# Kernel tuning notes

Hardware: AMD Instinct MI355X
Metric: run time of the kernel (lower is better)

The kernel has to match this reference:

```python
import jax, jax.numpy as jnp
import numpy as np

N = 50000          # nodes
E = 1000000        # edges
EMB = 64           # emb_dim
L = 3              # num_layer
B = 250            # graphs (200 nodes each)
XF, EF = 7, 5      # node / edge feature dims
BN_EPS = 1e-5


def setup_inputs() -> dict:
    key = jax.random.key(0)
    ks = jax.random.split(key, 16)
    x = jax.random.normal(ks[0], (N, XF), dtype=jnp.float32)
    edge_attr = jax.random.normal(ks[1], (E, EF), dtype=jnp.float32)
    edge_index = jax.random.randint(ks[2], (2, E), 0, N, dtype=jnp.int32)
    # 250 contiguous graphs of 200 nodes: last node index of each graph
    last_idx = jnp.arange(1, B + 1, dtype=jnp.int32) * (N // B) - 1
    s = 0.05
    xW = jax.random.normal(ks[3], (XF, EMB), dtype=jnp.float32) * s
    xb = jnp.zeros((EMB,), dtype=jnp.float32)
    eW = jax.random.normal(ks[4], (L, EF, EMB), dtype=jnp.float32) * s
    eb = jnp.zeros((L, EMB), dtype=jnp.float32)
    W1 = jax.random.normal(ks[5], (L, EMB, 2 * EMB), dtype=jnp.float32) * s
    b1 = jnp.zeros((L, 2 * EMB), dtype=jnp.float32)
    W2 = jax.random.normal(ks[6], (L, 2 * EMB, EMB), dtype=jnp.float32) * s
    b2 = jnp.zeros((L, EMB), dtype=jnp.float32)
    gamma = jnp.ones((L, EMB), dtype=jnp.float32)
    beta = jnp.zeros((L, EMB), dtype=jnp.float32)
    return {"x": x, "edge_attr": edge_attr, "edge_index": edge_index,
            "last_idx": last_idx, "xW": xW, "xb": xb, "eW": eW, "eb": eb,
            "W1": W1, "b1": b1, "W2": W2, "b2": b2,
            "gamma": gamma, "beta": beta}


def _gnn_forward(x, edge_attr, edge_index, last_idx, xW, xb, eW, eb, W1, b1, W2, b2, gamma, beta):
    n = x.shape[0]
    # self-loop edge attrs: first column = 8, rest 0
    self_attr = jnp.zeros((n, EF), dtype=edge_attr.dtype).at[:, 0].set(8.0)
    ea = jnp.concatenate([edge_attr, self_attr], axis=0)          # [E+N, EF]
    loop = jnp.arange(n, dtype=edge_index.dtype)
    src = jnp.concatenate([edge_index[0], loop])                  # x_j indices
    dst = jnp.concatenate([edge_index[1], loop])                  # aggregation targets

    h = x @ xW + xb                                               # [N, EMB]
    for l in range(L):
        e = ea @ eW[l] + eb[l]                                    # [E+N, EMB]
        msg = h[src] + e                                          # gather + combine
        agg = jax.ops.segment_sum(msg, dst, num_segments=n)       # scatter-add
        h2 = jax.nn.relu(agg @ W1[l] + b1[l]) @ W2[l] + b2[l]     # GIN MLP
        mean = jnp.mean(h2, axis=0)
        var = jnp.mean(jnp.square(h2 - mean), axis=0)             # biased, like torch BN
        hn = (h2 - mean) * jax.lax.rsqrt(var + BN_EPS) * gamma[l] + beta[l]
        h = jax.nn.elu(hn) if l < L - 1 else hn                   # drop_ratio = 0
    return h[last_idx]                                            # super-node reps [B, EMB]


def reference(x, edge_attr, edge_index, last_idx, xW, xb, eW, eb, W1, b1, W2, b2, gamma, beta):
    return _gnn_forward(x, edge_attr, edge_index, last_idx, xW, xb, eW, eb, W1, b1, W2, b2, gamma, beta)
```

## Files before the change

kernel.cpp:

```cpp
#include <hip/hip_runtime.h>

#define N_NODES 50000
#define N_EDGES 1000000
#define EMB     64
#define HID     128
#define NLAYER  3
#define NGRAPH  250
#define XFD     7
#define EFD     5
#define BN_EPS  1e-5f

#define BKT_SH 8
#define BKT_SZ 256
#define NBKT   ((N_NODES + BKT_SZ - 1) / BKT_SZ)
#define CHKE   4096
#define NCHK   ((N_EDGES + CHKE - 1) / CHKE)
#define CNTM   (NBKT * NCHK)
#define NB2    ((CNTM + 255) / 256)

typedef short bf8_t __attribute__((ext_vector_type(8)));
typedef float f4_t  __attribute__((ext_vector_type(4)));

union FragU {
    uint4 q;
    bf8_t v;
    unsigned short u[8];
};

__device__ __forceinline__ void atomAddF(float* p, float v) {
    __hip_atomic_fetch_add(p, v, __ATOMIC_RELAXED, __HIP_MEMORY_SCOPE_AGENT);
}

__device__ __forceinline__ unsigned short f2bf(float f) {
    unsigned int u = __float_as_uint(f);
    u += 0x7fffu + ((u >> 16) & 1u);
    return (unsigned short)(u >> 16);
}
__device__ __forceinline__ float bf2f(unsigned short s) {
    return __uint_as_float(((unsigned int)s) << 16);
}
__device__ __forceinline__ float4 bf4(ushort4 u) {
    return make_float4(bf2f(u.x), bf2f(u.y), bf2f(u.z), bf2f(u.w));
}

__global__ void k_input(const float* __restrict__ x, const float* __restrict__ xW,
                        const float* __restrict__ xb, unsigned short* __restrict__ h) {
    int gid = blockIdx.x * 256 + threadIdx.x;
    if (gid >= (N_NODES + 1) * EMB) return;
    int n = gid >> 6, f = gid & 63;
    if (n == N_NODES) { h[gid] = 0; return; }
    float acc = xb[f];
#pragma unroll
    for (int k = 0; k < XFD; ++k) acc = fmaf(x[n * XFD + k], xW[k * EMB + f], acc);
    h[gid] = f2bf(acc);
}

__global__ void k_packW(const float* __restrict__ W1, const float* __restrict__ W2,
                        unsigned short* __restrict__ pw1, unsigned short* __restrict__ pw2) {
    int gid = blockIdx.x * 256 + threadIdx.x;
    int layer = gid >> 14;
    int r = gid & 16383;
    if (layer >= NLAYER) return;
    if (r < 8192) {
        int p = r;
        int j = p & 7, lane = (p >> 3) & 63, ts = p >> 9;
        int t = ts >> 1, s = ts & 1;
        int k = 32 * s + 8 * (lane >> 4) + j;
        int n = 16 * t + (lane & 15);
        pw1[layer * 8192 + p] = f2bf(W1[layer * EMB * HID + k * HID + n]);
    } else {
        int p = r - 8192;
        int j = p & 7, lane = (p >> 3) & 63, ts = p >> 9;
        int t = ts >> 2, s = ts & 3;
        int k = 32 * s + 8 * (lane >> 4) + j;
        int n = 16 * t + (lane & 15);
        pw2[layer * 8192 + p] = f2bf(W2[layer * HID * EMB + k * EMB + n]);
    }
}

__global__ __launch_bounds__(256) void k_binA(const int* __restrict__ dst,
                                              int* __restrict__ cntmat) {
    __shared__ int hist[NBKT];
    int tid = threadIdx.x, c = blockIdx.x;
    for (int i = tid; i < NBKT; i += 256) hist[i] = 0;
    __syncthreads();
    int e0 = c * CHKE, e1 = min(e0 + CHKE, N_EDGES);
    for (int i = e0 + tid; i < e1; i += 256) atomicAdd(&hist[dst[i] >> BKT_SH], 1);
    __syncthreads();
    for (int b = tid; b < NBKT; b += 256) cntmat[b * NCHK + c] = hist[b];
}

__global__ __launch_bounds__(256) void k_gscanA(const int* __restrict__ in, int n,
                                                int* __restrict__ bsum) {
    int tid = threadIdx.x, lane = tid & 63, wid = tid >> 6;
    int i = blockIdx.x * 256 + tid;
    int v = (i < n) ? in[i] : 0;
#pragma unroll
    for (int off = 32; off; off >>= 1) v += __shfl_down(v, off);
    __shared__ int ws[4];
    if (lane == 0) ws[wid] = v;
    __syncthreads();
    if (tid == 0) bsum[blockIdx.x] = ws[0] + ws[1] + ws[2] + ws[3];
}

__global__ __launch_bounds__(256) void k_gscanB(const int* __restrict__ bsum, int nb,
                                                int* __restrict__ boff) {
    int tid = threadIdx.x, lane = tid & 63, wid = tid >> 6;
    int v = (tid < nb) ? bsum[tid] : 0;
    int x = v;
#pragma unroll
    for (int off = 1; off < 64; off <<= 1) {
        int y = __shfl_up(x, off);
        if (lane >= off) x += y;
    }
    __shared__ int wtot[4];
    if (lane == 63) wtot[wid] = x;
    __syncthreads();
    int woff = 0;
    for (int w = 0; w < wid; ++w) woff += wtot[w];
    if (tid < nb) boff[tid] = woff + x - v;
}

__global__ __launch_bounds__(256) void k_gscanC(const int* __restrict__ in, int n,
                                                const int* __restrict__ boff,
                                                int* __restrict__ out) {
    int tid = threadIdx.x, lane = tid & 63, wid = tid >> 6;
    int i = blockIdx.x * 256 + tid;
    int v = (i < n) ? in[i] : 0;
    int x = v;
#pragma unroll
    for (int off = 1; off < 64; off <<= 1) {
        int y = __shfl_up(x, off);
        if (lane >= off) x += y;
    }
    __shared__ int wtot[4];
    if (lane == 63) wtot[wid] = x;
    __syncthreads();
    int woff = boff[blockIdx.x];
    for (int w = 0; w < wid; ++w) woff += wtot[w];
    if (i < n) out[i] = woff + x - v;
}

__global__ __launch_bounds__(256) void k_binC(const int* __restrict__ src,
                                              const int* __restrict__ dst,
                                              const int* __restrict__ off2,
                                              int2* __restrict__ bufSD) {
    __shared__ int cur[NBKT];
    int tid = threadIdx.x, c = blockIdx.x;
    for (int b = tid; b < NBKT; b += 256) cur[b] = off2[b * NCHK + c];
    __syncthreads();
    int e0 = c * CHKE, e1 = min(e0 + CHKE, N_EDGES);
    for (int i = e0 + tid; i < e1; i += 256) {
        int d = dst[i];
        int b = d >> BKT_SH;
        int p = atomicAdd(&cur[b], 1);
        bufSD[p] = make_int2(src[i], ((d & (BKT_SZ - 1)) << 20) | i);
    }
}

__global__ __launch_bounds__(256) void k_binD(const int2* __restrict__ bufSD,
                                              const int* __restrict__ off2,
                                              int* __restrict__ csr,
                                              int* __restrict__ csrE,
                                              int* __restrict__ rowstart) {
    __shared__ int hist[BKT_SZ];
    __shared__ int cur[BKT_SZ];
    __shared__ int wtot[4];
    int tid = threadIdx.x, b = blockIdx.x;
    int bstart = off2[b * NCHK];
    int bend = (b + 1 < NBKT) ? off2[(b + 1) * NCHK] : N_EDGES;
    hist[tid] = 0;
    __syncthreads();
    for (int j = bstart + tid; j < bend; j += 256)
        atomicAdd(&hist[bufSD[j].y >> 20], 1);
    __syncthreads();
    int lane = tid & 63, wid = tid >> 6;
    int v = hist[tid], x = v;
#pragma unroll
    for (int off = 1; off < 64; off <<= 1) {
        int y = __shfl_up(x, off);
        if (lane >= off) x += y;
    }
    if (lane == 63) wtot[wid] = x;
    __syncthreads();
    int woff = 0;
    for (int w = 0; w < wid; ++w) woff += wtot[w];
    int ex = woff + x - v;
    cur[tid] = ex;
    int node = b * BKT_SZ + tid;
    if (node < N_NODES) rowstart[node] = bstart + ex;
    if (b == NBKT - 1 && tid == 0) rowstart[N_NODES] = N_EDGES;
    __syncthreads();
    for (int j = bstart + tid; j < bend; j += 256) {
        int2 t = bufSD[j];
        int local = t.y >> 20;
        int p = atomicAdd(&cur[local], 1);
        csr[bstart + p] = t.x;
        csrE[bstart + p] = t.y & 0xFFFFF;
    }
}

__global__ __launch_bounds__(256) void k_aggE(const int* __restrict__ rowstart,
                                              const int* __restrict__ csrE,
                                              const float* __restrict__ ea,
                                              float* __restrict__ aggE) {
    int wave = (blockIdx.x * 256 + threadIdx.x) >> 6;
    int lane = threadIdx.x & 63;
    int g = lane >> 4, l15 = lane & 15;
    int n = wave * 4 + g;
    if (n >= N_NODES) return;
    int j0 = rowstart[n], j1 = rowstart[n + 1];
    float s0 = 0.f, s1 = 0.f, s2 = 0.f, s3 = 0.f, s4 = 0.f;
    for (int j = j0 + l15; j < j1; j += 16) {
        int e = csrE[j];
        const float* p = ea + (size_t)e * EFD;
        s0 += p[0]; s1 += p[1]; s2 += p[2]; s3 += p[3]; s4 += p[4];
    }
#pragma unroll
    for (int off = 1; off < 16; off <<= 1) {
        s0 += __shfl_xor(s0, off);
        s1 += __shfl_xor(s1, off);
        s2 += __shfl_xor(s2, off);
        s3 += __shfl_xor(s3, off);
        s4 += __shfl_xor(s4, off);
    }
    if (l15 < 5) {
        float v = (l15 == 0) ? s0 : (l15 == 1) ? s1 : (l15 == 2) ? s2
                : (l15 == 3) ? s3 : s4;
        aggE[(size_t)n * EFD + l15] = v;
    }
}

#define ACC8(v)                                                         \
    do {                                                                \
        f0 += __uint_as_float((v).x << 16);                             \
        f1 += __uint_as_float((v).x & 0xffff0000u);                     \
        f2 += __uint_as_float((v).y << 16);                             \
        f3 += __uint_as_float((v).y & 0xffff0000u);                     \
        f4 += __uint_as_float((v).z << 16);                             \
        f5 += __uint_as_float((v).z & 0xffff0000u);                     \
        f6 += __uint_as_float((v).w << 16);                             \
        f7 += __uint_as_float((v).w & 0xffff0000u);                     \
    } while (0)

__global__ __launch_bounds__(256) void k_agg(const unsigned short* __restrict__ h,
                                             float* __restrict__ agg,
                                             const int* __restrict__ rowstart,
                                             const int* __restrict__ csr,
                                             const float* __restrict__ aggE,
                                             const float* __restrict__ eWl,
                                             const float* __restrict__ ebl) {
    int wave = (blockIdx.x * 256 + threadIdx.x) >> 6;
    int lane = threadIdx.x & 63;
    int nbase = wave * 4;
    if (nbase >= N_NODES) return;
    int lg3 = lane >> 3, lq3 = lane & 7;
    int lg = lane >> 4, lq = lane & 15;
    const uint4* hb8 = (const uint4*)h;
    const ushort4* hb4 = (const ushort4*)h;
    const float4* eW4 = (const float4*)eWl;
    float4 ew0 = eW4[lq], ew1 = eW4[16 + lq], ew2 = eW4[32 + lq],
           ew3 = eW4[48 + lq], ew4 = eW4[64 + lq];
    float4 eb4 = ((const float4*)ebl)[lq];
    int nend = min(nbase + 4, N_NODES);
    for (int n = nbase; n < nend; ++n) {
        int j0 = rowstart[n], j1 = rowstart[n + 1];
        float f0 = 0.f, f1 = 0.f, f2 = 0.f, f3 = 0.f,
              f4 = 0.f, f5 = 0.f, f6 = 0.f, f7 = 0.f;
        for (int j = j0; j < j1;) {
            int take = j1 - j;
            if (take > 64) take = 64;
            int myid = (lane < take) ? csr[j + lane] : N_NODES;
            int s0 = __shfl(myid, lg3);
            int s1 = __shfl(myid, 8 + lg3);
            int s2 = __shfl(myid, 16 + lg3);
            int s3 = __shfl(myid, 24 + lg3);
            uint4 v0 = hb8[(size_t)s0 * 8 + lq3];
            uint4 v1 = hb8[(size_t)s1 * 8 + lq3];
            uint4 v2 = hb8[(size_t)s2 * 8 + lq3];
            uint4 v3 = hb8[(size_t)s3 * 8 + lq3];
            ACC8(v0); ACC8(v1); ACC8(v2); ACC8(v3);
            if (take > 32) {
                int s4 = __shfl(myid, 32 + lg3);
                int s5 = __shfl(myid, 40 + lg3);
                int s6 = __shfl(myid, 48 + lg3);
                int s7 = __shfl(myid, 56 + lg3);
                uint4 w0 = hb8[(size_t)s4 * 8 + lq3];
                uint4 w1 = hb8[(size_t)s5 * 8 + lq3];
                uint4 w2 = hb8[(size_t)s6 * 8 + lq3];
                uint4 w3 = hb8[(size_t)s7 * 8 + lq3];
                ACC8(w0); ACC8(w1); ACC8(w2); ACC8(w3);
            }
            j += take;
        }
#define RED8(F)                     \
        F += __shfl_xor(F, 8);      \
        F += __shfl_xor(F, 16);     \
        F += __shfl_xor(F, 32);
        RED8(f0) RED8(f1) RED8(f2) RED8(f3) RED8(f4) RED8(f5) RED8(f6) RED8(f7)
#undef RED8
        int srcl = lq >> 1;
        float x0 = __shfl(f0, srcl), x4 = __shfl(f4, srcl);
        float x1 = __shfl(f1, srcl), x5 = __shfl(f5, srcl);
        float x2 = __shfl(f2, srcl), x6 = __shfl(f6, srcl);
        float x3 = __shfl(f3, srcl), x7 = __shfl(f7, srcl);
        bool hiHalf = (lq & 1) != 0;
        float4 acc;
        acc.x = hiHalf ? x4 : x0;
        acc.y = hiHalf ? x5 : x1;
        acc.z = hiHalf ? x6 : x2;
        acc.w = hiHalf ? x7 : x3;
        float a0 = aggE[n * 5 + 0], a1 = aggE[n * 5 + 1], a2 = aggE[n * 5 + 2],
              a3 = aggE[n * 5 + 3], a4 = aggE[n * 5 + 4];
        float c0 = a0 + 8.f;
        float ce = (float)(j1 - j0) + 1.f;
        float4 bb = bf4(hb4[(size_t)n * 16 + lq]);
        bb.x = fmaf(c0, ew0.x, bb.x); bb.y = fmaf(c0, ew0.y, bb.y);
        bb.z = fmaf(c0, ew0.z, bb.z); bb.w = fmaf(c0, ew0.w, bb.w);
        bb.x = fmaf(a1, ew1.x, bb.x); bb.y = fmaf(a1, ew1.y, bb.y);
        bb.z = fmaf(a1, ew1.z, bb.z); bb.w = fmaf(a1, ew1.w, bb.w);
        bb.x = fmaf(a2, ew2.x, bb.x); bb.y = fmaf(a2, ew2.y, bb.y);
        bb.z = fmaf(a2, ew2.z, bb.z); bb.w = fmaf(a2, ew2.w, bb.w);
        bb.x = fmaf(a3, ew3.x, bb.x); bb.y = fmaf(a3, ew3.y, bb.y);
        bb.z = fmaf(a3, ew3.z, bb.z); bb.w = fmaf(a3, ew3.w, bb.w);
        bb.x = fmaf(a4, ew4.x, bb.x); bb.y = fmaf(a4, ew4.y, bb.y);
        bb.z = fmaf(a4, ew4.z, bb.z); bb.w = fmaf(a4, ew4.w, bb.w);
        bb.x = fmaf(ce, eb4.x, bb.x); bb.y = fmaf(ce, eb4.y, bb.y);
        bb.z = fmaf(ce, eb4.z, bb.z); bb.w = fmaf(ce, eb4.w, bb.w);
        if (lg == 0) {
            ((float4*)agg)[(size_t)n * 16 + lq] =
                make_float4(acc.x + bb.x, acc.y + bb.y, acc.z + bb.z, acc.w + bb.w);
        }
    }
}
#undef ACC8

__global__ __launch_bounds__(256) void k_mlp(const float* __restrict__ agg,
                                             float* __restrict__ h2,
                                             const unsigned short* __restrict__ pw1,
                                             const float* __restrict__ b1l,
                                             const unsigned short* __restrict__ pw2,
                                             const float* __restrict__ b2l,
                                             float* __restrict__ stats) {
    __shared__ __align__(16) unsigned short hid[64 * 136];
    int tid = threadIdx.x;
    int w = tid >> 6, lane = tid & 63;
    int q = lane >> 4, l15 = lane & 15;
    int n0 = blockIdx.x * 64;
    int mrow = n0 + 16 * w + l15;
    const float* arow = agg + (size_t)(mrow < N_NODES ? mrow : N_NODES - 1) * EMB;
    FragU fa[2];
#pragma unroll
    for (int s = 0; s < 2; ++s) {
        float4 x0 = *(const float4*)&arow[32 * s + 8 * q];
        float4 x1 = *(const float4*)&arow[32 * s + 8 * q + 4];
        fa[s].u[0] = f2bf(x0.x); fa[s].u[1] = f2bf(x0.y);
        fa[s].u[2] = f2bf(x0.z); fa[s].u[3] = f2bf(x0.w);
        fa[s].u[4] = f2bf(x1.x); fa[s].u[5] = f2bf(x1.y);
        fa[s].u[6] = f2bf(x1.z); fa[s].u[7] = f2bf(x1.w);
    }
    const uint4* w1f = (const uint4*)pw1;
    f4_t acc1[8];
#pragma unroll
    for (int t = 0; t < 8; ++t) {
        acc1[t] = (f4_t){0.f, 0.f, 0.f, 0.f};
        FragU b0, b1;
        b0.q = w1f[(t * 2 + 0) * 64 + lane];
        b1.q = w1f[(t * 2 + 1) * 64 + lane];
        acc1[t] = __builtin_amdgcn_mfma_f32_16x16x32_bf16(fa[0].v, b0.v, acc1[t], 0, 0, 0);
        acc1[t] = __builtin_amdgcn_mfma_f32_16x16x32_bf16(fa[1].v, b1.v, acc1[t], 0, 0, 0);
    }
#pragma unroll
    for (int t = 0; t < 8; ++t) {
        int col = 16 * t + l15;
        float bv = b1l[col];
#pragma unroll
        for (int r = 0; r < 4; ++r) {
            int m = 16 * w + q * 4 + r;
            hid[m * 136 + col] = f2bf(fmaxf(acc1[t][r] + bv, 0.f));
        }
    }
    FragU fa2[4];
#pragma unroll
    for (int s = 0; s < 4; ++s)
        fa2[s].q = *(const uint4*)&hid[(16 * w + l15) * 136 + 32 * s + 8 * q];
    const uint4* w2f = (const uint4*)pw2;
    f4_t acc2[4];
#pragma unroll
    for (int t = 0; t < 4; ++t) {
        acc2[t] = (f4_t){0.f, 0.f, 0.f, 0.f};
#pragma unroll
        for (int s = 0; s < 4; ++s) {
            FragU b;
            b.q = w2f[(t * 4 + s) * 64 + lane];
            acc2[t] = __builtin_amdgcn_mfma_f32_16x16x32_bf16(fa2[s].v, b.v, acc2[t], 0, 0, 0);
        }
    }
    float sacc[4] = {0.f, 0.f, 0.f, 0.f}, qacc[4] = {0.f, 0.f, 0.f, 0.f};
#pragma unroll
    for (int t = 0; t < 4; ++t) {
        int col = 16 * t + l15;
        float bv = b2l[col];
#pragma unroll
        for (int r = 0; r < 4; ++r) {
            int nn = n0 + 16 * w + q * 4 + r;
            if (nn < N_NODES) {
                float v = acc2[t][r] + bv;
                h2[(size_t)nn * EMB + col] = v;
                sacc[t] += v;
                qacc[t] = fmaf(v, v, qacc[t]);
            }
        }
    }
#pragma unroll
    for (int t = 0; t < 4; ++t) {
        sacc[t] += __shfl_xor(sacc[t], 16); qacc[t] += __shfl_xor(qacc[t], 16);
        sacc[t] += __shfl_xor(sacc[t], 32); qacc[t] += __shfl_xor(qacc[t], 32);
    }
    __syncthreads();
    float* red = (float*)hid;
    if (q == 0) {
#pragma unroll
        for (int t = 0; t < 4; ++t) {
            red[w * 64 + 16 * t + l15] = sacc[t];
            red[256 + w * 64 + 16 * t + l15] = qacc[t];
        }
    }
    __syncthreads();
    if (tid < 64) {
        float s = red[tid] + red[64 + tid] + red[128 + tid] + red[192 + tid];
        float qq = red[256 + tid] + red[320 + tid] + red[384 + tid] + red[448 + tid];
        atomAddF(&stats[tid], s);
        atomAddF(&stats[64 + tid], qq);
    }
}

__global__ void k_bn(const float* __restrict__ h2, unsigned short* __restrict__ h,
                     const float* __restrict__ stats, const float* __restrict__ gam,
                     const float* __restrict__ bet) {
    int gid = blockIdx.x * 256 + threadIdx.x;
    if (gid >= N_NODES * EMB) return;
    int f = gid & 63;
    const float invN = 1.f / (float)N_NODES;
    float mean = stats[f] * invN;
    float var = stats[64 + f] * invN - mean * mean;
    float inv = rsqrtf(var + BN_EPS);
    float v = (h2[gid] - mean) * inv * gam[f] + bet[f];
    h[gid] = f2bf(v > 0.f ? v : expm1f(v));
}

__global__ void k_bnout(const float* __restrict__ h2, const int* __restrict__ last,
                        const float* __restrict__ stats, const float* __restrict__ gam,
                        const float* __restrict__ bet, float* __restrict__ out) {
    int gid = blockIdx.x * 256 + threadIdx.x;
    if (gid >= NGRAPH * EMB) return;
    int b = gid >> 6, f = gid & 63;
    const float invN = 1.f / (float)N_NODES;
    float mean = stats[f] * invN;
    float var = stats[64 + f] * invN - mean * mean;
    float inv = rsqrtf(var + BN_EPS);
    out[gid] = (h2[last[b] * EMB + f] - mean) * inv * gam[f] + bet[f];
}

extern "C" void kernel_launch(void* const* d_in, const int* in_sizes, int n_in,
                              void* d_out, int out_size, void* d_ws, size_t ws_size,
                              hipStream_t stream) {
    const float* x   = (const float*)d_in[0];
    const float* ea  = (const float*)d_in[1];
    const int*   eidx= (const int*)d_in[2];
    const int*   last= (const int*)d_in[3];
    const float* xW  = (const float*)d_in[4];
    const float* xb  = (const float*)d_in[5];
    const float* eW  = (const float*)d_in[6];
    const float* eb  = (const float*)d_in[7];
    const float* W1  = (const float*)d_in[8];
    const float* b1  = (const float*)d_in[9];
    const float* W2  = (const float*)d_in[10];
    const float* b2  = (const float*)d_in[11];
    const float* gam = (const float*)d_in[12];
    const float* bet = (const float*)d_in[13];
    float* out = (float*)d_out;

    const int* srcI = eidx;
    const int* dstI = eidx + N_EDGES;

    float* hslot  = (float*)d_ws;
    float* agg    = hslot + (N_NODES + 1) * EMB;
    float* aggE   = agg + N_NODES * EMB;
    float* stats  = aggE + NBKT * BKT_SZ * EFD;
    int* rowstart = (int*)(stats + NLAYER * 2 * EMB);
    int* csr      = rowstart + N_NODES + 1;
    int* csrE     = csr + N_EDGES;
    int* cntmat   = csrE + N_EDGES;
    int* off2     = cntmat + CNTM;
    int* bsum     = off2 + CNTM;
    int* boff     = bsum + NB2;
    unsigned short* pw1 = (unsigned short*)(boff + NB2);
    unsigned short* pw2 = pw1 + NLAYER * EMB * HID;
    unsigned short* h = (unsigned short*)hslot;
    int2* bufSD   = (int2*)agg;

    hipMemsetAsync(stats, 0, NLAYER * 2 * EMB * sizeof(float), stream);

    k_input<<<((N_NODES + 1) * EMB + 255) / 256, 256, 0, stream>>>(x, xW, xb, h);
    k_packW<<<(NLAYER * 2 * EMB * HID + 255) / 256, 256, 0, stream>>>(W1, W2, pw1, pw2);
    k_binA<<<NCHK, 256, 0, stream>>>(dstI, cntmat);
    k_gscanA<<<NB2, 256, 0, stream>>>(cntmat, CNTM, bsum);
    k_gscanB<<<1, 256, 0, stream>>>(bsum, NB2, boff);
    k_gscanC<<<NB2, 256, 0, stream>>>(cntmat, CNTM, boff, off2);
    k_binC<<<NCHK, 256, 0, stream>>>(srcI, dstI, off2, bufSD);
    k_binD<<<NBKT, 256, 0, stream>>>(bufSD, off2, csr, csrE, rowstart);
    k_aggE<<<(N_NODES / 4 * 64 + 255) / 256, 256, 0, stream>>>(rowstart, csrE, ea, aggE);

    const int aggBlocks = ((N_NODES + 3) / 4 * 64 + 255) / 256;
    const int mlpBlocks = (N_NODES + 63) / 64;
    for (int l = 0; l < NLAYER; ++l) {
        k_agg<<<aggBlocks, 256, 0, stream>>>(
            h, agg, rowstart, csr, aggE, eW + l * EFD * EMB, eb + l * EMB);
        k_mlp<<<mlpBlocks, 256, 0, stream>>>(agg, agg, pw1 + l * EMB * HID, b1 + l * HID,
                                             pw2 + l * HID * EMB, b2 + l * EMB,
                                             stats + l * 2 * EMB);
        if (l < NLAYER - 1) {
            k_bn<<<(N_NODES * EMB + 255) / 256, 256, 0, stream>>>(
                agg, h, stats + l * 2 * EMB, gam + l * EMB, bet + l * EMB);
        } else {
            k_bnout<<<(NGRAPH * EMB + 255) / 256, 256, 0, stream>>>(
                agg, last, stats + l * 2 * EMB, gam + l * EMB, bet + l * EMB, out);
        }
    }
}
```

Before: 357.3 us.

## Fuse prep kernels, single-block scan, and fold edge-attr aggregation into layer-0 agg

Merges input projection, weight packing and stats zeroing into one k_prep launch, and replaces the three-kernel global scan with a single 1024-thread block scan. The separate edge-attribute aggregation kernel is removed; its work now happens inside the first-layer k_agg through a template flag. Nodes per wave in k_agg drop from 4 to 2 for more parallelism. The aim is fewer kernel launches and one less pass over csrE. The trade-off is a serial single-block scan and extra gather and reduction work inside layer 0.

```diff
diff --git a/kernel.cpp b/kernel.cpp
--- a/kernel.cpp
+++ b/kernel.cpp
@@ -16,7 +16,8 @@
 #define CHKE   4096
 #define NCHK   ((N_EDGES + CHKE - 1) / CHKE)
 #define CNTM   (NBKT * NCHK)
-#define NB2    ((CNTM + 255) / 256)
+#define INPB   ((((N_NODES + 1) * EMB) + 255) / 256)
+#define PACKB  ((NLAYER * 2 * EMB * HID + 255) / 256)
 
 typedef short bf8_t __attribute__((ext_vector_type(8)));
 typedef float f4_t  __attribute__((ext_vector_type(4)));
@@ -43,38 +44,43 @@
     return make_float4(bf2f(u.x), bf2f(u.y), bf2f(u.z), bf2f(u.w));
 }
 
-__global__ void k_input(const float* __restrict__ x, const float* __restrict__ xW,
-                        const float* __restrict__ xb, unsigned short* __restrict__ h) {
-    int gid = blockIdx.x * 256 + threadIdx.x;
-    if (gid >= (N_NODES + 1) * EMB) return;
-    int n = gid >> 6, f = gid & 63;
-    if (n == N_NODES) { h[gid] = 0; return; }
-    float acc = xb[f];
-#pragma unroll
-    for (int k = 0; k < XFD; ++k) acc = fmaf(x[n * XFD + k], xW[k * EMB + f], acc);
-    h[gid] = f2bf(acc);
-}
-
-__global__ void k_packW(const float* __restrict__ W1, const float* __restrict__ W2,
-                        unsigned short* __restrict__ pw1, unsigned short* __restrict__ pw2) {
-    int gid = blockIdx.x * 256 + threadIdx.x;
-    int layer = gid >> 14;
-    int r = gid & 16383;
-    if (layer >= NLAYER) return;
-    if (r < 8192) {
-        int p = r;
-        int j = p & 7, lane = (p >> 3) & 63, ts = p >> 9;
-        int t = ts >> 1, s = ts & 1;
-        int k = 32 * s + 8 * (lane >> 4) + j;
-        int n = 16 * t + (lane & 15);
-        pw1[layer * 8192 + p] = f2bf(W1[layer * EMB * HID + k * HID + n]);
+__global__ void k_prep(const float* __restrict__ x, const float* __restrict__ xW,
+                       const float* __restrict__ xb, unsigned short* __restrict__ h,
+                       const float* __restrict__ W1, const float* __restrict__ W2,
+                       unsigned short* __restrict__ pw1, unsigned short* __restrict__ pw2,
+                       float* __restrict__ stats) {
+    int bid = blockIdx.x;
+    if (bid < INPB) {
+        int gid = bid * 256 + threadIdx.x;
+        if (gid >= (N_NODES + 1) * EMB) return;
+        int n = gid >> 6, f = gid & 63;
+        if (n == N_NODES) { h[gid] = 0; return; }
+        float acc = xb[f];
+#pragma unroll
+        for (int k = 0; k < XFD; ++k) acc = fmaf(x[n * XFD + k], xW[k * EMB + f], acc);
+        h[gid] = f2bf(acc);
+    } else if (bid < INPB + PACKB) {
+        int gid = (bid - INPB) * 256 + threadIdx.x;
+        int layer = gid >> 14;
+        int r = gid & 16383;
+        if (layer >= NLAYER) return;
+        if (r < 8192) {
+            int p = r;
+            int j = p & 7, lane = (p >> 3) & 63, ts = p >> 9;
+            int t = ts >> 1, s = ts & 1;
+            int k = 32 * s + 8 * (lane >> 4) + j;
+            int n = 16 * t + (lane & 15);
+            pw1[layer * 8192 + p] = f2bf(W1[layer * EMB * HID + k * HID + n]);
+        } else {
+            int p = r - 8192;
+            int j = p & 7, lane = (p >> 3) & 63, ts = p >> 9;
+            int t = ts >> 2, s = ts & 3;
+            int k = 32 * s + 8 * (lane >> 4) + j;
+            int n = 16 * t + (lane & 15);
+            pw2[layer * 8192 + p] = f2bf(W2[layer * HID * EMB + k * EMB + n]);
+        }
     } else {
-        int p = r - 8192;
-        int j = p & 7, lane = (p >> 3) & 63, ts = p >> 9;
-        int t = ts >> 2, s = ts & 3;
-        int k = 32 * s + 8 * (lane >> 4) + j;
-        int n = 16 * t + (lane & 15);
-        pw2[layer * 8192 + p] = f2bf(W2[layer * HID * EMB + k * EMB + n]);
+        for (int i = threadIdx.x; i < NLAYER * 2 * EMB; i += 256) stats[i] = 0.f;
     }
 }
 
@@ -90,55 +96,33 @@
     for (int b = tid; b < NBKT; b += 256) cntmat[b * NCHK + c] = hist[b];
 }
 
-__global__ __launch_bounds__(256) void k_gscanA(const int* __restrict__ in, int n,
-                                                int* __restrict__ bsum) {
+__global__ __launch_bounds__(1024) void k_scan(const int* __restrict__ in,
+                                               int* __restrict__ out) {
+    __shared__ int wsum[16];
     int tid = threadIdx.x, lane = tid & 63, wid = tid >> 6;
-    int i = blockIdx.x * 256 + tid;
-    int v = (i < n) ? in[i] : 0;
-#pragma unroll
-    for (int off = 32; off; off >>= 1) v += __shfl_down(v, off);
-    __shared__ int ws[4];
-    if (lane == 0) ws[wid] = v;
-    __syncthreads();
-    if (tid == 0) bsum[blockIdx.x] = ws[0] + ws[1] + ws[2] + ws[3];
-}
-
-__global__ __launch_bounds__(256) void k_gscanB(const int* __restrict__ bsum, int nb,
-                                                int* __restrict__ boff) {
-    int tid = threadIdx.x, lane = tid & 63, wid = tid >> 6;
-    int v = (tid < nb) ? bsum[tid] : 0;
-    int x = v;
-#pragma unroll
-    for (int off = 1; off < 64; off <<= 1) {
-        int y = __shfl_up(x, off);
-        if (lane >= off) x += y;
-    }
-    __shared__ int wtot[4];
-    if (lane == 63) wtot[wid] = x;
-    __syncthreads();
-    int woff = 0;
-    for (int w = 0; w < wid; ++w) woff += wtot[w];
-    if (tid < nb) boff[tid] = woff + x - v;
-}
-
-__global__ __launch_bounds__(256) void k_gscanC(const int* __restrict__ in, int n,
-                                                const int* __restrict__ boff,
-                                                int* __restrict__ out) {
-    int tid = threadIdx.x, lane = tid & 63, wid = tid >> 6;
-    int i = blockIdx.x * 256 + tid;
-    int v = (i < n) ? in[i] : 0;
-    int x = v;
-#pragma unroll
-    for (int off = 1; off < 64; off <<= 1) {
-        int y = __shfl_up(x, off);
-        if (lane >= off) x += y;
-    }
-    __shared__ int wtot[4];
-    if (lane == 63) wtot[wid] = x;
-    __syncthreads();
-    int woff = boff[blockIdx.x];
-    for (int w = 0; w < wid; ++w) woff += wtot[w];
-    if (i < n) out[i] = woff + x - v;
+    int carry = 0;
+    for (int base = 0; base < CNTM; base += 1024) {
+        int i = base + tid;
+        int v = (i < CNTM) ? in[i] : 0;
+        int x = v;
+#pragma unroll
+        for (int off = 1; off < 64; off <<= 1) {
+            int y = __shfl_up(x, off);
+            if (lane >= off) x += y;
+        }
+        if (lane == 63) wsum[wid] = x;
+        __syncthreads();
+        int woff = 0, tot = 0;
+#pragma unroll
+        for (int w = 0; w < 16; ++w) {
+            int s = wsum[w];
+            if (w < wid) woff += s;
+            tot += s;
+        }
+        if (i < CNTM) out[i] = carry + woff + x - v;
+        carry += tot;
+        __syncthreads();
+    }
 }
 
 __global__ __launch_bounds__(256) void k_binC(const int* __restrict__ src,
@@ -200,37 +184,6 @@
     }
 }
 
-__global__ __launch_bounds__(256) void k_aggE(const int* __restrict__ rowstart,
-                                              const int* __restrict__ csrE,
-                                              const float* __restrict__ ea,
-                                              float* __restrict__ aggE) {
-    int wave = (blockIdx.x * 256 + threadIdx.x) >> 6;
-    int lane = threadIdx.x & 63;
-    int g = lane >> 4, l15 = lane & 15;
-    int n = wave * 4 + g;
-    if (n >= N_NODES) return;
-    int j0 = rowstart[n], j1 = rowstart[n + 1];
-    float s0 = 0.f, s1 = 0.f, s2 = 0.f, s3 = 0.f, s4 = 0.f;
-    for (int j = j0 + l15; j < j1; j += 16) {
-        int e = csrE[j];
-        const float* p = ea + (size_t)e * EFD;
-        s0 += p[0]; s1 += p[1]; s2 += p[2]; s3 += p[3]; s4 += p[4];
-    }
-#pragma unroll
-    for (int off = 1; off < 16; off <<= 1) {
-        s0 += __shfl_xor(s0, off);
-        s1 += __shfl_xor(s1, off);
-        s2 += __shfl_xor(s2, off);
-        s3 += __shfl_xor(s3, off);
-        s4 += __shfl_xor(s4, off);
-    }
-    if (l15 < 5) {
-        float v = (l15 == 0) ? s0 : (l15 == 1) ? s1 : (l15 == 2) ? s2
-                : (l15 == 3) ? s3 : s4;
-        aggE[(size_t)n * EFD + l15] = v;
-    }
-}
-
 #define ACC8(v)                                                         \
     do {                                                                \
         f0 += __uint_as_float((v).x << 16);                             \
@@ -243,16 +196,19 @@
         f7 += __uint_as_float((v).w & 0xffff0000u);                     \
     } while (0)
 
+template <int L0>
 __global__ __launch_bounds__(256) void k_agg(const unsigned short* __restrict__ h,
                                              float* __restrict__ agg,
                                              const int* __restrict__ rowstart,
                                              const int* __restrict__ csr,
-                                             const float* __restrict__ aggE,
+                                             const int* __restrict__ csrE,
+                                             const float* __restrict__ ea,
+                                             float* __restrict__ aggE,
                                              const float* __restrict__ eWl,
                                              const float* __restrict__ ebl) {
     int wave = (blockIdx.x * 256 + threadIdx.x) >> 6;
     int lane = threadIdx.x & 63;
-    int nbase = wave * 4;
+    int nbase = wave * 2;
     if (nbase >= N_NODES) return;
     int lg3 = lane >> 3, lq3 = lane & 7;
     int lg = lane >> 4, lq = lane & 15;
@@ -262,15 +218,22 @@
     float4 ew0 = eW4[lq], ew1 = eW4[16 + lq], ew2 = eW4[32 + lq],
            ew3 = eW4[48 + lq], ew4 = eW4[64 + lq];
     float4 eb4 = ((const float4*)ebl)[lq];
-    int nend = min(nbase + 4, N_NODES);
+    int nend = min(nbase + 2, N_NODES);
     for (int n = nbase; n < nend; ++n) {
         int j0 = rowstart[n], j1 = rowstart[n + 1];
         float f0 = 0.f, f1 = 0.f, f2 = 0.f, f3 = 0.f,
               f4 = 0.f, f5 = 0.f, f6 = 0.f, f7 = 0.f;
+        float e0 = 0.f, e1 = 0.f, e2 = 0.f, e3 = 0.f, e4 = 0.f;
         for (int j = j0; j < j1;) {
             int take = j1 - j;
             if (take > 64) take = 64;
             int myid = (lane < take) ? csr[j + lane] : N_NODES;
+            if (L0) {
+                if (lane < take) {
+                    const float* p = ea + (size_t)csrE[j + lane] * EFD;
+                    e0 += p[0]; e1 += p[1]; e2 += p[2]; e3 += p[3]; e4 += p[4];
+                }
+            }
             int s0 = __shfl(myid, lg3);
             int s1 = __shfl(myid, 8 + lg3);
             int s2 = __shfl(myid, 16 + lg3);
@@ -299,6 +262,26 @@
         F += __shfl_xor(F, 32);
         RED8(f0) RED8(f1) RED8(f2) RED8(f3) RED8(f4) RED8(f5) RED8(f6) RED8(f7)
 #undef RED8
+        float a0, a1, a2, a3, a4;
+        if (L0) {
+#pragma unroll
+            for (int off = 1; off < 64; off <<= 1) {
+                e0 += __shfl_xor(e0, off);
+                e1 += __shfl_xor(e1, off);
+                e2 += __shfl_xor(e2, off);
+                e3 += __shfl_xor(e3, off);
+                e4 += __shfl_xor(e4, off);
+            }
+            a0 = e0; a1 = e1; a2 = e2; a3 = e3; a4 = e4;
+            if (lane < EFD) {
+                float v = (lane == 0) ? e0 : (lane == 1) ? e1 : (lane == 2) ? e2
+                        : (lane == 3) ? e3 : e4;
+                aggE[(size_t)n * EFD + lane] = v;
+            }
+        } else {
+            a0 = aggE[n * 5 + 0]; a1 = aggE[n * 5 + 1]; a2 = aggE[n * 5 + 2];
+            a3 = aggE[n * 5 + 3]; a4 = aggE[n * 5 + 4];
+        }
         int srcl = lq >> 1;
         float x0 = __shfl(f0, srcl), x4 = __shfl(f4, srcl);
         float x1 = __shfl(f1, srcl), x5 = __shfl(f5, srcl);
@@ -310,8 +293,6 @@
         acc.y = hiHalf ? x5 : x1;
         acc.z = hiHalf ? x6 : x2;
         acc.w = hiHalf ? x7 : x3;
-        float a0 = aggE[n * 5 + 0], a1 = aggE[n * 5 + 1], a2 = aggE[n * 5 + 2],
-              a3 = aggE[n * 5 + 3], a4 = aggE[n * 5 + 4];
         float c0 = a0 + 8.f;
         float ce = (float)(j1 - j0) + 1.f;
         float4 bb = bf4(hb4[(size_t)n * 16 + lq]);
@@ -487,36 +468,32 @@
     float* hslot  = (float*)d_ws;
     float* agg    = hslot + (N_NODES + 1) * EMB;
     float* aggE   = agg + N_NODES * EMB;
-    float* stats  = aggE + NBKT * BKT_SZ * EFD;
+    float* stats  = aggE + N_NODES * EFD;
     int* rowstart = (int*)(stats + NLAYER * 2 * EMB);
     int* csr      = rowstart + N_NODES + 1;
     int* csrE     = csr + N_EDGES;
     int* cntmat   = csrE + N_EDGES;
     int* off2     = cntmat + CNTM;
-    int* bsum     = off2 + CNTM;
-    int* boff     = bsum + NB2;
-    unsigned short* pw1 = (unsigned short*)(boff + NB2);
+    unsigned short* pw1 = (unsigned short*)(off2 + CNTM);
     unsigned short* pw2 = pw1 + NLAYER * EMB * HID;
     unsigned short* h = (unsigned short*)hslot;
     int2* bufSD   = (int2*)agg;
 
-    hipMemsetAsync(stats, 0, NLAYER * 2 * EMB * sizeof(float), stream);
-
-    k_input<<<((N_NODES + 1) * EMB + 255) / 256, 256, 0, stream>>>(x, xW, xb, h);
-    k_packW<<<(NLAYER * 2 * EMB * HID + 255) / 256, 256, 0, stream>>>(W1, W2, pw1, pw2);
+    k_prep<<<INPB + PACKB + 1, 256, 0, stream>>>(x, xW, xb, h, W1, W2, pw1, pw2, stats);
     k_binA<<<NCHK, 256, 0, stream>>>(dstI, cntmat);
-    k_gscanA<<<NB2, 256, 0, stream>>>(cntmat, CNTM, bsum);
-    k_gscanB<<<1, 256, 0, stream>>>(bsum, NB2, boff);
-    k_gscanC<<<NB2, 256, 0, stream>>>(cntmat, CNTM, boff, off2);
+    k_scan<<<1, 1024, 0, stream>>>(cntmat, off2);
     k_binC<<<NCHK, 256, 0, stream>>>(srcI, dstI, off2, bufSD);
     k_binD<<<NBKT, 256, 0, stream>>>(bufSD, off2, csr, csrE, rowstart);
-    k_aggE<<<(N_NODES / 4 * 64 + 255) / 256, 256, 0, stream>>>(rowstart, csrE, ea, aggE);
-
-    const int aggBlocks = ((N_NODES + 3) / 4 * 64 + 255) / 256;
+
+    const int aggBlocks = ((N_NODES + 1) / 2 * 64 + 255) / 256;
     const int mlpBlocks = (N_NODES + 63) / 64;
     for (int l = 0; l < NLAYER; ++l) {
-        k_agg<<<aggBlocks, 256, 0, stream>>>(
-            h, agg, rowstart, csr, aggE, eW + l * EFD * EMB, eb + l * EMB);
+        if (l == 0)
+            k_agg<1><<<aggBlocks, 256, 0, stream>>>(
+                h, agg, rowstart, csr, csrE, ea, aggE, eW + l * EFD * EMB, eb + l * EMB);
+        else
+            k_agg<0><<<aggBlocks, 256, 0, stream>>>(
+                h, agg, rowstart, csr, csrE, ea, aggE, eW + l * EFD * EMB, eb + l * EMB);
         k_mlp<<<mlpBlocks, 256, 0, stream>>>(agg, agg, pw1 + l * EMB * HID, b1 + l * HID,
                                              pw2 + l * HID * EMB, b2 + l * EMB,
                                              stats + l * 2 * EMB);
```

Result: slower. 386.9 us (+8.3%).
